# Performance work log

Hardware: AMD Instinct MI355X
Metric: run time of the kernel (lower is better)

The kernel has to match this reference:

```python
import jax, jax.numpy as jnp
import numpy as np

B, T, D, HS = 8, 2048, 768, 64  # batch, seq, n_embd, head_size


def setup_inputs() -> dict:
    key = jax.random.key(0)
    kx, kq, kk, kv = jax.random.split(key, 4)
    scale = 1.0 / np.sqrt(D)
    return {
        "x": jax.random.normal(kx, (B, T, D), dtype=jnp.float32),
        "Wq": jax.random.normal(kq, (D, HS), dtype=jnp.float32) * scale,
        "Wk": jax.random.normal(kk, (D, HS), dtype=jnp.float32) * scale,
        "Wv": jax.random.normal(kv, (D, HS), dtype=jnp.float32) * scale,
    }


def reference(x, Wq, Wk, Wv):
    # q,k,v: [B,T,HS]
    q = jnp.einsum("btd,dh->bth", x, Wq)
    k = jnp.einsum("btd,dh->bth", x, Wk)
    v = jnp.einsum("btd,dh->bth", x, Wv)
    hs = k.shape[-1]
    # scaled scores: [B,T,T]
    wei = jnp.einsum("bth,bsh->bts", q, k) * (hs ** -0.5)
    # causal mask (lower-triangular keeps, upper -> -inf)
    causal = jnp.tril(jnp.ones((x.shape[1], x.shape[1]), dtype=bool))
    wei = jnp.where(causal[None, :, :], wei, -jnp.inf)
    wei = jax.nn.softmax(wei, axis=-1)
    return jnp.einsum("bts,bsh->bth", wei, v)
```

## Files before the change

kernel.cpp:

```cpp
#include <hip/hip_runtime.h>

typedef float  f32x4  __attribute__((ext_vector_type(4)));
typedef short  short8 __attribute__((ext_vector_type(8)));
typedef short  short4_ __attribute__((ext_vector_type(4)));

constexpr int Bb = 8, T = 2048, D = 768, HS = 64;
constexpr int BT = Bb * T;
constexpr int QT = T / 64;
constexpr int PSTRIDE = 64 * 64 + 128;

__device__ __forceinline__ short f2bf(float f) {
    unsigned u = __builtin_bit_cast(unsigned, f);
    unsigned r = (u + 0x7FFFu + ((u >> 16) & 1u)) >> 16;
    return (short)r;
}

__device__ __forceinline__ void gld_lds16(const void* g, void* l) {
    __builtin_amdgcn_global_load_lds(
        (const __attribute__((address_space(1))) unsigned int*)g,
        (__attribute__((address_space(3))) unsigned int*)l, 16, 0, 0);
}

__global__ __launch_bounds__(256) void wt_kernel(const float* __restrict__ Wq,
                                                 const float* __restrict__ Wk,
                                                 const float* __restrict__ Wv,
                                                 short* __restrict__ Wt) {
    int n = blockIdx.x;
    const float* W = (n < 64) ? Wq : (n < 128) ? Wk : Wv;
    int c = n & 63;
    for (int kk = threadIdx.x; kk < D; kk += 256)
        Wt[n * D + kk] = f2bf(W[kk * HS + c]);
}

__global__ __launch_bounds__(512) void qkv_proj(const float* __restrict__ x,
                                                const short* __restrict__ Wt,
                                                short* __restrict__ qws,
                                                short* __restrict__ kws,
                                                short* __restrict__ vtg) {
    __shared__ alignas(16) short wtile[3][192 * 64];
    __shared__ alignas(16) float xls[3][64 * 64];

    const int tid  = threadIdx.x;
    const int lane = tid & 63, w = tid >> 6;
    const int lo   = lane & 15, hi = lane >> 4;
    const int wr   = w >> 2, wc = w & 3;
    const int row0 = blockIdx.x * 64;
    const int b    = row0 >> 11, t0 = row0 & 2047;

    f32x4 acc[6];
#pragma unroll
    for (int j = 0; j < 6; j++) acc[j] = f32x4{0.f, 0.f, 0.f, 0.f};

#define STAGE_W(bufi, kc)                                                      \
    {                                                                          \
        _Pragma("unroll")                                                      \
        for (int it = 0; it < 3; it++) {                                       \
            int ci = it * 512 + w * 64 + lane;                                 \
            int n = ci >> 3, seg = ci & 7;                                     \
            gld_lds16(&Wt[(size_t)n * D + (kc) * 64 + ((seg ^ (n & 7)) << 3)], \
                      &wtile[bufi][(it * 512 + w * 64) * 8]);                  \
        }                                                                      \
    }
#define STAGE_X(bufi, kc)                                                      \
    {                                                                          \
        _Pragma("unroll")                                                      \
        for (int it = 0; it < 2; it++) {                                       \
            int idx = it * 512 + tid;                                          \
            int row = idx >> 4, g = idx & 15;                                  \
            int sg = (g & 8) | ((g & 7) ^ (row & 7));                          \
            gld_lds16(&x[(size_t)(row0 + row) * D + (kc) * 64 + sg * 4],       \
                      &xls[bufi][(it * 512 + w * 64) * 4]);                    \
        }                                                                      \
    }

    STAGE_W(0, 0); STAGE_X(0, 0);
    STAGE_W(1, 1); STAGE_X(1, 1);
    STAGE_W(2, 2); STAGE_X(2, 2);

#pragma unroll
    for (int kc = 0; kc < 12; kc++) {
        if (kc <= 9)       asm volatile("s_waitcnt vmcnt(10)" ::: "memory");
        else if (kc == 10) asm volatile("s_waitcnt vmcnt(5)" ::: "memory");
        else               asm volatile("s_waitcnt vmcnt(0)" ::: "memory");
        __builtin_amdgcn_s_barrier();
        __builtin_amdgcn_sched_barrier(0);

        const int buf = kc % 3;
#pragma unroll
        for (int m = 0; m < 2; m++) {
            const int row = wr * 32 + m * 16 + lo;
            const int rg  = row & 7;
            float4 f00 = *reinterpret_cast<const float4*>(
                &xls[buf][row * 64 + (((2 * hi) ^ rg)) * 4]);
            float4 f01 = *reinterpret_cast<const float4*>(
                &xls[buf][row * 64 + (((2 * hi + 1) ^ rg)) * 4]);
            float4 f10 = *reinterpret_cast<const float4*>(
                &xls[buf][row * 64 + (8 + ((2 * hi) ^ rg)) * 4]);
            float4 f11 = *reinterpret_cast<const float4*>(
                &xls[buf][row * 64 + (8 + ((2 * hi + 1) ^ rg)) * 4]);
            short8 a0, a1;
#pragma unroll
            for (int e = 0; e < 4; e++) {
                a0[e]     = f2bf(f00[e]);
                a0[e + 4] = f2bf(f01[e]);
                a1[e]     = f2bf(f10[e]);
                a1[e + 4] = f2bf(f11[e]);
            }
#pragma unroll
            for (int j = 0; j < 3; j++) {
                const int brow = wc * 48 + j * 16 + lo;
                const int rx   = (brow & 7) << 3;
                short8 b0 = *reinterpret_cast<const short8*>(
                    &wtile[buf][brow * 64 + ((hi << 3) ^ rx)]);
                short8 b1 = *reinterpret_cast<const short8*>(
                    &wtile[buf][brow * 64 + (((hi + 4) << 3) ^ rx)]);
                acc[m * 3 + j] = __builtin_amdgcn_mfma_f32_16x16x32_bf16(a0, b0, acc[m * 3 + j], 0, 0, 0);
                acc[m * 3 + j] = __builtin_amdgcn_mfma_f32_16x16x32_bf16(a1, b1, acc[m * 3 + j], 0, 0, 0);
            }
        }
        __builtin_amdgcn_sched_barrier(0);
        __builtin_amdgcn_s_barrier();
        if (kc <= 8) {
            STAGE_W(buf, kc + 3);
            STAGE_X(buf, kc + 3);
        }
    }
#undef STAGE_W
#undef STAGE_X

#pragma unroll
    for (int m = 0; m < 2; m++) {
        const int orow = row0 + wr * 32 + m * 16 + hi * 4;
#pragma unroll
        for (int j = 0; j < 3; j++) {
            const int cb = wc * 48 + j * 16;
            const f32x4 a = acc[m * 3 + j];
            if (cb < 64) {
#pragma unroll
                for (int r = 0; r < 4; r++)
                    qws[(size_t)(orow + r) * HS + cb + lo] = f2bf(a[r] * 0.125f);
            } else if (cb < 128) {
#pragma unroll
                for (int r = 0; r < 4; r++)
                    kws[(size_t)(orow + r) * HS + cb - 64 + lo] = f2bf(a[r]);
            } else {
                short4_ pv;
#pragma unroll
                for (int r = 0; r < 4; r++) pv[r] = f2bf(a[r]);
                *reinterpret_cast<short4_*>(
                    &vtg[((size_t)b * 64 + cb - 128 + lo) * T + t0 + wr * 32 + m * 16 + hi * 4]) = pv;
            }
        }
    }
}

__global__ __launch_bounds__(256, 4) void attn(const short* __restrict__ qg,
                                               const short* __restrict__ kg,
                                               const short* __restrict__ vtg,
                                               float* __restrict__ part, int S) {
    __shared__ short ks[2][64 * 64];
    __shared__ short vts[2][64 * 64];
    __shared__ short ps[4][16 * 64];

    const int tid  = threadIdx.x;
    const int lane = tid & 63, w = tid >> 6;
    const int lo   = lane & 15, hi = lane >> 4;
    const int bid  = blockIdx.x;
    const int per_b = QT * S;
    const int b    = bid / per_b;
    const int r2   = bid % per_b;
    const int qt   = 31 - (r2 / S);
    const int c    = r2 % S;
    const int nkt  = qt + 1;
    const int base = nkt / S, rem = nkt % S;
    const int niter = base + (c < rem ? 1 : 0);
    const int kt0   = c * base + (c < rem ? c : rem);
    float* pout = part + (size_t)((b * QT + qt) * S + c) * PSTRIDE;

    float m_ = -1e30f;
    f32x4 lac = f32x4{0.f, 0.f, 0.f, 0.f};
    f32x4 oacc[4];
#pragma unroll
    for (int i = 0; i < 4; i++) oacc[i] = f32x4{0.f, 0.f, 0.f, 0.f};

    if (niter > 0) {
        const int qrow = qt * 64 + w * 16 + lo;
        const size_t qbase = ((size_t)b * T + qrow) * HS;
        short8 qa0 = *reinterpret_cast<const short8*>(&qg[qbase + hi * 8]);
        short8 qa1 = *reinterpret_cast<const short8*>(&qg[qbase + 32 + hi * 8]);

        const int srow = tid >> 2, scs = tid & 3, r7 = srow & 7;
        const int w0 = srow * 64 + (((scs * 2)     ^ r7) << 3);
        const int w1 = srow * 64 + (((scs * 2 + 1) ^ r7) << 3);
        const size_t kgoff = (size_t)b * T * HS;
        const size_t vgoff = ((size_t)b * 64 + srow) * T;

        short8 ka, kb2, va, vb;
        {
            const short* kp = &kg[kgoff + (size_t)(kt0 * 64 + srow) * HS + scs * 16];
            ka = *reinterpret_cast<const short8*>(kp);
            kb2 = *reinterpret_cast<const short8*>(kp + 8);
            const short* vp = &vtg[vgoff + kt0 * 64 + scs * 16];
            va = *reinterpret_cast<const short8*>(vp);
            vb = *reinterpret_cast<const short8*>(vp + 8);
        }
        *reinterpret_cast<short8*>(&ks[0][w0])  = ka;
        *reinterpret_cast<short8*>(&ks[0][w1])  = kb2;
        *reinterpret_cast<short8*>(&vts[0][w0]) = va;
        *reinterpret_cast<short8*>(&vts[0][w1]) = vb;

        const int pswz = (lo & 7) << 3;
        int cur = 0;
        for (int i = 0; i < niter; i++) {
            const int kt = kt0 + i;
            if (i + 1 < niter) {
                const short* kp = &kg[kgoff + (size_t)((kt + 1) * 64 + srow) * HS + scs * 16];
                ka = *reinterpret_cast<const short8*>(kp);
                kb2 = *reinterpret_cast<const short8*>(kp + 8);
                const short* vp = &vtg[vgoff + (kt + 1) * 64 + scs * 16];
                va = *reinterpret_cast<const short8*>(vp);
                vb = *reinterpret_cast<const short8*>(vp + 8);
            }
            __syncthreads();

            f32x4 sacc[4];
#pragma unroll
            for (int nt = 0; nt < 4; nt++) sacc[nt] = f32x4{0.f, 0.f, 0.f, 0.f};
            __builtin_amdgcn_s_setprio(1);
#pragma unroll
            for (int nt = 0; nt < 4; nt++) {
                const int row = nt * 16 + lo, rr = row & 7;
                short8 b0 = *reinterpret_cast<const short8*>(
                    &ks[cur][row * 64 + ((hi ^ rr) << 3)]);
                short8 b1 = *reinterpret_cast<const short8*>(
                    &ks[cur][row * 64 + (((hi + 4) ^ rr) << 3)]);
                sacc[nt] = __builtin_amdgcn_mfma_f32_16x16x32_bf16(b0, qa0, sacc[nt], 0, 0, 0);
                sacc[nt] = __builtin_amdgcn_mfma_f32_16x16x32_bf16(b1, qa1, sacc[nt], 0, 0, 0);
            }
            __builtin_amdgcn_s_setprio(0);

            if (kt == qt) {
#pragma unroll
                for (int nt = 0; nt < 4; nt++)
#pragma unroll
                    for (int r = 0; r < 4; r++)
                        if (nt * 16 + hi * 4 + r > w * 16 + lo) sacc[nt][r] = -1e30f;
            }

            float tm = fmaxf(fmaxf(fmaxf(sacc[0][0], sacc[0][1]), fmaxf(sacc[0][2], sacc[0][3])),
                             fmaxf(fmaxf(sacc[1][0], sacc[1][1]), fmaxf(sacc[1][2], sacc[1][3])));
            tm = fmaxf(tm, fmaxf(fmaxf(fmaxf(sacc[2][0], sacc[2][1]), fmaxf(sacc[2][2], sacc[2][3])),
                                 fmaxf(fmaxf(sacc[3][0], sacc[3][1]), fmaxf(sacc[3][2], sacc[3][3]))));
            tm = fmaxf(tm, __shfl_xor(tm, 16));
            tm = fmaxf(tm, __shfl_xor(tm, 32));

            if (!__all(tm <= m_ + 8.0f)) {
                float mnew = fmaxf(m_, tm);
                float corr = __expf(m_ - mnew);
#pragma unroll
                for (int r = 0; r < 4; r++) lac[r] *= corr;
#pragma unroll
                for (int r = 0; r < 4; r++) {
                    float cr = __shfl(corr, (lane & 48) | (hi * 4 + r));
#pragma unroll
                    for (int nt = 0; nt < 4; nt++) oacc[nt][r] *= cr;
                }
                m_ = mnew;
            }

#pragma unroll
            for (int nt = 0; nt < 4; nt++) {
                float p0 = __expf(sacc[nt][0] - m_);
                float p1 = __expf(sacc[nt][1] - m_);
                float p2 = __expf(sacc[nt][2] - m_);
                float p3 = __expf(sacc[nt][3] - m_);
                lac[0] += p0; lac[1] += p1; lac[2] += p2; lac[3] += p3;
                short4_ pk;
                pk[0] = f2bf(p0); pk[1] = f2bf(p1);
                pk[2] = f2bf(p2); pk[3] = f2bf(p3);
                *reinterpret_cast<short4_*>(
                    &ps[w][lo * 64 + ((nt * 16 + hi * 4) ^ pswz)]) = pk;
            }
            asm volatile("" ::: "memory");

            short8 pa0 = *reinterpret_cast<const short8*>(
                &ps[w][lo * 64 + ((hi << 3) ^ pswz)]);
            short8 pa1 = *reinterpret_cast<const short8*>(
                &ps[w][lo * 64 + (((hi + 4) << 3) ^ pswz)]);
            __builtin_amdgcn_s_setprio(1);
#pragma unroll
            for (int nt = 0; nt < 4; nt++) {
                const int row = nt * 16 + lo, rr = row & 7;
                short8 b0 = *reinterpret_cast<const short8*>(
                    &vts[cur][row * 64 + ((hi ^ rr) << 3)]);
                short8 b1 = *reinterpret_cast<const short8*>(
                    &vts[cur][row * 64 + (((hi + 4) ^ rr) << 3)]);
                oacc[nt] = __builtin_amdgcn_mfma_f32_16x16x32_bf16(pa0, b0, oacc[nt], 0, 0, 0);
                oacc[nt] = __builtin_amdgcn_mfma_f32_16x16x32_bf16(pa1, b1, oacc[nt], 0, 0, 0);
            }
            __builtin_amdgcn_s_setprio(0);

            if (i + 1 < niter) {
                *reinterpret_cast<short8*>(&ks[cur ^ 1][w0])  = ka;
                *reinterpret_cast<short8*>(&ks[cur ^ 1][w1])  = kb2;
                *reinterpret_cast<short8*>(&vts[cur ^ 1][w0]) = va;
                *reinterpret_cast<short8*>(&vts[cur ^ 1][w1]) = vb;
            }
            cur ^= 1;
        }
    }

    float l_ = (lac[0] + lac[1]) + (lac[2] + lac[3]);
    float lt = l_;
    lt += __shfl_xor(lt, 16);
    lt += __shfl_xor(lt, 32);

#pragma unroll
    for (int nt = 0; nt < 4; nt++)
#pragma unroll
        for (int r = 0; r < 4; r++)
            pout[(w * 16 + hi * 4 + r) * 64 + nt * 16 + lo] = oacc[nt][r];
    float mfor[4], lfor[4];
#pragma unroll
    for (int r = 0; r < 4; r++) {
        mfor[r] = __shfl(m_, (lane & 48) | (hi * 4 + r));
        lfor[r] = __shfl(lt, (lane & 48) | (hi * 4 + r));
    }
    if (lo == 0) {
#pragma unroll
        for (int r = 0; r < 4; r++) {
            const int row = w * 16 + hi * 4 + r;
            pout[4096 + row] = mfor[r];
            pout[4160 + row] = lfor[r];
        }
    }
}

__global__ __launch_bounds__(256) void combine(const float* __restrict__ part,
                                               float* __restrict__ out, int S) {
    const int bid = blockIdx.x;
    const int b = bid >> 5, qt = bid & 31;
    const float* p = part + (size_t)bid * S * PSTRIDE;
    const int row = threadIdx.x >> 2, cs = threadIdx.x & 3;

    float mv[4], lv[4], av[4];
    float M = -1e30f;
    for (int s = 0; s < S; s++) {
        mv[s] = p[(size_t)s * PSTRIDE + 4096 + row];
        lv[s] = p[(size_t)s * PSTRIDE + 4160 + row];
        M = fmaxf(M, mv[s]);
    }
    float den = 0.0f;
    for (int s = 0; s < S; s++) { av[s] = __expf(mv[s] - M); den += lv[s] * av[s]; }
    float inv = 1.0f / den;

    float* o = out + ((size_t)b * T + qt * 64 + row) * HS + cs * 16;
#pragma unroll
    for (int i = 0; i < 4; i++) {
        float4 res = make_float4(0.f, 0.f, 0.f, 0.f);
        for (int s = 0; s < S; s++) {
            float4 v = *reinterpret_cast<const float4*>(
                p + (size_t)s * PSTRIDE + row * 64 + cs * 16 + i * 4);
            res.x += v.x * av[s]; res.y += v.y * av[s];
            res.z += v.z * av[s]; res.w += v.w * av[s];
        }
        res.x *= inv; res.y *= inv; res.z *= inv; res.w *= inv;
        *reinterpret_cast<float4*>(o + i * 4) = res;
    }
}

extern "C" void kernel_launch(void* const* d_in, const int* in_sizes, int n_in,
                              void* d_out, int out_size, void* d_ws, size_t ws_size,
                              hipStream_t stream) {
    const float* x  = (const float*)d_in[0];
    const float* Wq = (const float*)d_in[1];
    const float* Wk = (const float*)d_in[2];
    const float* Wv = (const float*)d_in[3];
    float* out = (float*)d_out;

    short* ws   = (short*)d_ws;
    short* qws  = ws;
    short* kws  = qws + (size_t)BT * HS;
    short* vtws = kws + (size_t)BT * HS;
    short* Wt   = vtws + (size_t)BT * HS;
    float* part = (float*)(Wt + (size_t)192 * D);

    const size_t fixed = (size_t)3 * BT * HS * 2 + (size_t)192 * D * 2;
    int S = 4;
    while (S > 1 && fixed + (size_t)Bb * QT * S * PSTRIDE * 4 > ws_size) S >>= 1;

    wt_kernel<<<192, 256, 0, stream>>>(Wq, Wk, Wv, Wt);
    qkv_proj<<<BT / 64, 512, 0, stream>>>(x, Wt, qws, kws, vtws);
    attn<<<Bb * QT * S, 256, 0, stream>>>(qws, kws, vtws, part, S);
    combine<<<Bb * QT, 256, 0, stream>>>(part, out, S);
}
```

Before: 52.91 us.

## Single-buffer K/V LDS tiles and raise attention split to six for occupancy

Drops double-buffering of the K and V shared-memory tiles and adds a second barrier before writing the next tile, roughly halving LDS use per block. The launch bound moves to 6 blocks per CU, and the key-split factor S rises from 4 to 6, with the combine arrays enlarged to hold up to 8 partials. The aim is more resident waves and more parallel blocks to hide latency. The cost is an extra barrier per iteration, less overlap between writing the next tile and computing on the current one, and more partial output traffic for the combine step.

New measurement: 69.83 us. +32.0%, slower.

```diff
diff --git a/kernel.cpp b/kernel.cpp
--- a/kernel.cpp
+++ b/kernel.cpp
@@ -154,12 +154,12 @@
     }
 }
 
-__global__ __launch_bounds__(256, 4) void attn(const short* __restrict__ qg,
+__global__ __launch_bounds__(256, 6) void attn(const short* __restrict__ qg,
                                                const short* __restrict__ kg,
                                                const short* __restrict__ vtg,
                                                float* __restrict__ part, int S) {
-    __shared__ short ks[2][64 * 64];
-    __shared__ short vts[2][64 * 64];
+    __shared__ short ks[64 * 64];
+    __shared__ short vts[64 * 64];
     __shared__ short ps[4][16 * 64];
 
     const int tid  = threadIdx.x;
@@ -204,13 +204,12 @@
             va = *reinterpret_cast<const short8*>(vp);
             vb = *reinterpret_cast<const short8*>(vp + 8);
         }
-        *reinterpret_cast<short8*>(&ks[0][w0])  = ka;
-        *reinterpret_cast<short8*>(&ks[0][w1])  = kb2;
-        *reinterpret_cast<short8*>(&vts[0][w0]) = va;
-        *reinterpret_cast<short8*>(&vts[0][w1]) = vb;
+        *reinterpret_cast<short8*>(&ks[w0])  = ka;
+        *reinterpret_cast<short8*>(&ks[w1])  = kb2;
+        *reinterpret_cast<short8*>(&vts[w0]) = va;
+        *reinterpret_cast<short8*>(&vts[w1]) = vb;
 
         const int pswz = (lo & 7) << 3;
-        int cur = 0;
         for (int i = 0; i < niter; i++) {
             const int kt = kt0 + i;
             if (i + 1 < niter) {
@@ -231,9 +230,9 @@
             for (int nt = 0; nt < 4; nt++) {
                 const int row = nt * 16 + lo, rr = row & 7;
                 short8 b0 = *reinterpret_cast<const short8*>(
-                    &ks[cur][row * 64 + ((hi ^ rr) << 3)]);
+                    &ks[row * 64 + ((hi ^ rr) << 3)]);
                 short8 b1 = *reinterpret_cast<const short8*>(
-                    &ks[cur][row * 64 + (((hi + 4) ^ rr) << 3)]);
+                    &ks[row * 64 + (((hi + 4) ^ rr) << 3)]);
                 sacc[nt] = __builtin_amdgcn_mfma_f32_16x16x32_bf16(b0, qa0, sacc[nt], 0, 0, 0);
                 sacc[nt] = __builtin_amdgcn_mfma_f32_16x16x32_bf16(b1, qa1, sacc[nt], 0, 0, 0);
             }
@@ -292,21 +291,21 @@
             for (int nt = 0; nt < 4; nt++) {
                 const int row = nt * 16 + lo, rr = row & 7;
                 short8 b0 = *reinterpret_cast<const short8*>(
-                    &vts[cur][row * 64 + ((hi ^ rr) << 3)]);
+                    &vts[row * 64 + ((hi ^ rr) << 3)]);
                 short8 b1 = *reinterpret_cast<const short8*>(
-                    &vts[cur][row * 64 + (((hi + 4) ^ rr) << 3)]);
+                    &vts[row * 64 + (((hi + 4) ^ rr) << 3)]);
                 oacc[nt] = __builtin_amdgcn_mfma_f32_16x16x32_bf16(pa0, b0, oacc[nt], 0, 0, 0);
                 oacc[nt] = __builtin_amdgcn_mfma_f32_16x16x32_bf16(pa1, b1, oacc[nt], 0, 0, 0);
             }
             __builtin_amdgcn_s_setprio(0);
 
+            __syncthreads();
             if (i + 1 < niter) {
-                *reinterpret_cast<short8*>(&ks[cur ^ 1][w0])  = ka;
-                *reinterpret_cast<short8*>(&ks[cur ^ 1][w1])  = kb2;
-                *reinterpret_cast<short8*>(&vts[cur ^ 1][w0]) = va;
-                *reinterpret_cast<short8*>(&vts[cur ^ 1][w1]) = vb;
-            }
-            cur ^= 1;
+                *reinterpret_cast<short8*>(&ks[w0])  = ka;
+                *reinterpret_cast<short8*>(&ks[w1])  = kb2;
+                *reinterpret_cast<short8*>(&vts[w0]) = va;
+                *reinterpret_cast<short8*>(&vts[w1]) = vb;
+            }
         }
     }
 
@@ -343,7 +342,7 @@
     const float* p = part + (size_t)bid * S * PSTRIDE;
     const int row = threadIdx.x >> 2, cs = threadIdx.x & 3;
 
-    float mv[4], lv[4], av[4];
+    float mv[8], lv[8], av[8];
     float M = -1e30f;
     for (int s = 0; s < S; s++) {
         mv[s] = p[(size_t)s * PSTRIDE + 4096 + row];
@@ -386,8 +385,8 @@
     float* part = (float*)(Wt + (size_t)192 * D);
 
     const size_t fixed = (size_t)3 * BT * HS * 2 + (size_t)192 * D * 2;
-    int S = 4;
-    while (S > 1 && fixed + (size_t)Bb * QT * S * PSTRIDE * 4 > ws_size) S >>= 1;
+    int S = 6;
+    while (S > 1 && fixed + (size_t)Bb * QT * S * PSTRIDE * 4 > ws_size) S--;
 
     wt_kernel<<<192, 256, 0, stream>>>(Wq, Wk, Wv, Wt);
     qkv_proj<<<BT / 64, 512, 0, stream>>>(x, Wt, qws, kws, vtws);
```
